# Kernel optimization log

Hardware: AMD Instinct MI355X
Metric: run time of the kernel (lower is better)

Reference implementation:

```python
import jax, jax.numpy as jnp
import numpy as np

N = 20000      # nodes
E = 320000     # edges (avg degree 16)
IN = 64        # input feature dim
EMB = 128      # emb_dim / c_dim
OUT = 10       # num classes
L = 5          # num_layers
RATIO = 0.25
TEMP = 1.0
NOISE = 1.0
MAX_ITER = 30
EPS = 1e-20


def setup_inputs() -> dict:
    key = jax.random.key(0)
    ks = jax.random.split(key, 12)
    def w(k, shape, fan):
        return jax.random.normal(k, shape, jnp.float32) / np.float32(np.sqrt(fan))
    x = jax.random.normal(ks[0], (N, IN), jnp.float32)
    edge_index = jax.random.randint(ks[1], (2, E), 0, N, jnp.int32)
    u = jax.random.uniform(ks[2], (E, 1), jnp.float32)
    return {
        "x": x,
        "edge_index": edge_index,
        "u": u,
        "enc_W0": w(ks[3], (IN, EMB), IN), "enc_b0": jnp.zeros((EMB,), jnp.float32),
        "enc_W": w(ks[4], (L - 1, EMB, EMB), EMB), "enc_b": jnp.zeros((L - 1, EMB), jnp.float32),
        "ea_W1": w(ks[5], (2 * EMB, 4 * EMB), 2 * EMB), "ea_b1": jnp.zeros((4 * EMB,), jnp.float32),
        "ea_W2": w(ks[6], (4 * EMB, 1), 4 * EMB), "ea_b2": jnp.zeros((1,), jnp.float32),
        "cls_W0": w(ks[7], (IN, EMB), IN), "cls_b0": jnp.zeros((EMB,), jnp.float32),
        "cls_W": w(ks[8], (L - 1, EMB, EMB), EMB), "cls_b": jnp.zeros((L - 1, EMB), jnp.float32),
        "head_W": w(ks[9], (EMB, OUT), EMB), "head_b": jnp.zeros((OUT,), jnp.float32),
    }


def _gin_stack(x, W0, b0, Ws, bs, src, dst, att):
    """GIN-style stack: aggregate att-weighted neighbor messages, then linear+ReLU."""
    agg = jax.ops.segment_sum(x[src] * att, dst, num_segments=N)
    h = jax.nn.relu((x + agg) @ W0 + b0)
    def layer(h, wb):
        W, b = wb
        agg = jax.ops.segment_sum(h[src] * att, dst, num_segments=N)
        return jax.nn.relu((h + agg) @ W + b), None
    h, _ = jax.lax.scan(layer, h, (Ws, bs))
    return h


def reference(x, edge_index, u, enc_W0, enc_b0, enc_W, enc_b,
              ea_W1, ea_b1, ea_W2, ea_b2,
              cls_W0, cls_b0, cls_W, cls_b, head_W, head_b):
    src, dst = edge_index[0], edge_index[1]
    ones = jnp.ones((E, 1), jnp.float32)

    # GNN encoder
    h = _gin_stack(x, enc_W0, enc_b0, enc_W, enc_b, src, dst, ones)

    # edge attention MLP on [h_src, h_dst]
    edge_rep = jnp.concatenate([h[src], h[dst]], axis=-1)            # [E, 2*EMB]
    pe = jax.nn.relu(edge_rep @ ea_W1 + ea_b1) @ ea_W2 + ea_b2       # [E, 1]
    atts = (pe - pe.mean()) / jnp.std(pe, ddof=1)

    # Gumbel noise from uniform u (training path)
    g = -jnp.log(-jnp.log(u + EPS) + EPS)
    d = atts + g * NOISE

    s_min, s_max = atts.min(), atts.max()
    D = jnp.concatenate([d - s_min, s_max - d], axis=-1)             # [E, 2]
    logT = -D / TEMP
    log_rs = jnp.log(jnp.array([[E * (1.0 - RATIO), E * RATIO]], jnp.float32) + EPS)

    # 30-step Sinkhorn normalization in log space
    def body(i, lt):
        lt = lt - jax.scipy.special.logsumexp(lt, axis=-1, keepdims=True)
        lt = lt - jax.scipy.special.logsumexp(lt, axis=-2, keepdims=True)
        return lt + log_rs
    logT = jax.lax.fori_loop(0, MAX_ITER, body, logT)
    T = jnp.exp(logT)[:, 1:2]                                        # [E, 1]

    # classifier GNN on raw features with Sinkhorn edge attention
    hc = _gin_stack(x, cls_W0, cls_b0, cls_W, cls_b, src, dst, T)
    rep = hc.mean(axis=0)                                            # mean graph pooling
    return rep @ head_W + head_b                                     # [OUT]
```

## Files before the change

### kernel.cpp

```cpp
#include <hip/hip_runtime.h>
#include <math.h>

#define NN 20000
#define EE 320000
#define NBINS 2048
#define HRANGE 64.0f
#define EPSF 1e-20f

typedef __attribute__((ext_vector_type(8))) short bf16x8;
typedef __attribute__((ext_vector_type(4))) float f32x4;

constexpr size_t OFF_DEG  = 0;
constexpr size_t OFF_RS   = 20000;
constexpr size_t OFF_CUR  = 40008;
constexpr size_t OFF_EIX  = 60008;
constexpr size_t OFF_GSRC = 380008;
constexpr size_t OFF_B0   = 700008;
constexpr size_t OFF_B1   = 1980008;
constexpr size_t OFF_PA   = 3260008;
constexpr size_t OFF_PB   = 8380008;
constexpr size_t OFF_PE   = 13500008;
constexpr size_t OFF_DL   = 13820008;
constexpr size_t OFF_TT   = 14140008;
constexpr size_t OFF_HIST = 14460008;
constexpr size_t OFF_SCAL = 14464104;
constexpr size_t OFF_REP  = 14464136;
constexpr size_t OFF_WT   = 14464264;
constexpr size_t WT_ENC0 = 0;
constexpr size_t WT_ENC  = 8192;
constexpr size_t WT_CLS0 = 73728;
constexpr size_t WT_CLS  = 81920;
constexpr size_t WT_EA1  = 147456;

__device__ __forceinline__ unsigned ordf(float f) {
  unsigned b = __float_as_uint(f);
  return (b >> 31) ? ~b : (b | 0x80000000u);
}
__device__ __forceinline__ float unordf(unsigned u) {
  unsigned b = (u >> 31) ? (u ^ 0x80000000u) : ~u;
  return __uint_as_float(b);
}
__device__ __forceinline__ ushort f2bf(float f) {
  unsigned u = __float_as_uint(f);
  u += 0x7FFFu + ((u >> 16) & 1u);
  return (ushort)(u >> 16);
}
__device__ __forceinline__ unsigned pack2(float x, float y) {
  return (unsigned)f2bf(x) | ((unsigned)f2bf(y) << 16);
}
__device__ __forceinline__ float bf2f(ushort h) {
  return __uint_as_float(((unsigned)h) << 16);
}
__device__ __forceinline__ float bflo(unsigned v) { return __uint_as_float(v << 16); }
__device__ __forceinline__ float bfhi(unsigned v) { return __uint_as_float(v & 0xFFFF0000u); }

__global__ void init_ws(int* deg, int* cur, float* hist, float* scal, float* rep) {
  int i = blockIdx.x * blockDim.x + threadIdx.x;
  if (i < NN) { deg[i] = 0; cur[i] = 0; }
  if (i < 2 * NBINS) hist[i] = 0.f;
  if (i < 128) rep[i] = 0.f;
  if (i < 32) {
    if (i == 2)      ((unsigned*)scal)[2] = 0xFFFFFFFFu;
    else if (i == 3) ((unsigned*)scal)[3] = 0u;
    else scal[i] = 0.f;
  }
}

__global__ void count_deg(const int* __restrict__ dst, int* __restrict__ deg) {
  int e = blockIdx.x * 256 + threadIdx.x;
  if (e < EE) atomicAdd(&deg[dst[e]], 1);
}

__global__ __launch_bounds__(1024) void scan_deg(const int* __restrict__ deg,
                                                 int* __restrict__ rs) {
  __shared__ int ps[1024];
  const int t = threadIdx.x;
  const int base = t * 20;
  int loc[20];
  int s = 0;
#pragma unroll
  for (int j = 0; j < 20; ++j) {
    int idx = base + j;
    int v = (idx < NN) ? deg[idx] : 0;
    loc[j] = s;
    s += v;
  }
  ps[t] = s;
  __syncthreads();
  for (int off = 1; off < 1024; off <<= 1) {
    int x = (t >= off) ? ps[t - off] : 0;
    __syncthreads();
    ps[t] += x;
    __syncthreads();
  }
  const int excl = ps[t] - s;
#pragma unroll
  for (int j = 0; j < 20; ++j) {
    int idx = base + j;
    if (idx < NN) rs[idx] = excl + loc[j];
  }
  if (t == 1023) rs[NN] = ps[1023];
}

__global__ void fill_csr(const int* __restrict__ src, const int* __restrict__ dst,
                         const int* __restrict__ rs, int* __restrict__ cur,
                         int* __restrict__ eidx, int* __restrict__ gsrc) {
  int e = blockIdx.x * 256 + threadIdx.x;
  if (e < EE) {
    int d = dst[e];
    int p = atomicAdd(&cur[d], 1);
    int o = rs[d] + p;
    eidx[o] = e;
    gsrc[o] = src[e];
  }
}

__global__ void transpose_all(const float* __restrict__ encW0, const float* __restrict__ encW,
                              const float* __restrict__ clsW0, const float* __restrict__ clsW,
                              const float* __restrict__ eaW1, ushort* __restrict__ Wt) {
  int i = blockIdx.x * 256 + threadIdx.x;
  if (i < 8192) {
    int k = i >> 7, n = i & 127;
    Wt[WT_ENC0 + n * 64 + k] = f2bf(encW0[i]);
  } else if (i < 73728) {
    int j = i - 8192;
    int l = j >> 14, r = j & 16383, k = r >> 7, n = r & 127;
    Wt[WT_ENC + l * 16384 + n * 128 + k] = f2bf(encW[j]);
  } else if (i < 81920) {
    int j = i - 73728;
    int k = j >> 7, n = j & 127;
    Wt[WT_CLS0 + n * 64 + k] = f2bf(clsW0[j]);
  } else if (i < 147456) {
    int j = i - 81920;
    int l = j >> 14, r = j & 16383, k = r >> 7, n = r & 127;
    Wt[WT_CLS + l * 16384 + n * 128 + k] = f2bf(clsW[j]);
  } else if (i < 278528) {
    int j = i - 147456;
    int k = j >> 9, n = j & 511;
    Wt[WT_EA1 + n * 256 + k] = f2bf(eaW1[j]);
  }
}

template <bool HASATT>
__global__ __launch_bounds__(256) void fused_layer64(
    const float* __restrict__ X, ushort* __restrict__ C,
    const int* __restrict__ gsrc, const int* __restrict__ rs,
    const float* __restrict__ att, const ushort* __restrict__ Bt,
    const float* __restrict__ bias) {
  __shared__ __align__(16) char smem[16896];
  ushort* Asm = (ushort*)smem;
  const int tid = threadIdx.x;
  const int g = tid >> 3, l = tid & 7;
  const int nb = blockIdx.x * 32;
  {
    const int n = nb + g;
    const int e0 = rs[n], e1 = rs[n + 1];
    const float4* Xr = (const float4*)(X + (size_t)n * 64);
    float4 s0 = Xr[l * 2], s1 = Xr[l * 2 + 1];
    float a[8] = {s0.x, s0.y, s0.z, s0.w, s1.x, s1.y, s1.z, s1.w};
    int i = e0;
    float4 c0, c1, d0, d1;
    float cw = 1.f, dw = 1.f;
    if (i < e1) {
      const float4* R = (const float4*)(X + (size_t)gsrc[i] * 64);
      if (HASATT) cw = att[i];
      c0 = R[l * 2]; c1 = R[l * 2 + 1];
    }
    if (i + 1 < e1) {
      const float4* R = (const float4*)(X + (size_t)gsrc[i + 1] * 64);
      if (HASATT) dw = att[i + 1];
      d0 = R[l * 2]; d1 = R[l * 2 + 1];
    }
    while (i < e1) {
      float4 p0, p1;
      float pw = 1.f;
      if (i + 2 < e1) {
        const float4* R = (const float4*)(X + (size_t)gsrc[i + 2] * 64);
        if (HASATT) pw = att[i + 2];
        p0 = R[l * 2]; p1 = R[l * 2 + 1];
      }
      a[0] = fmaf(cw, c0.x, a[0]); a[1] = fmaf(cw, c0.y, a[1]);
      a[2] = fmaf(cw, c0.z, a[2]); a[3] = fmaf(cw, c0.w, a[3]);
      a[4] = fmaf(cw, c1.x, a[4]); a[5] = fmaf(cw, c1.y, a[5]);
      a[6] = fmaf(cw, c1.z, a[6]); a[7] = fmaf(cw, c1.w, a[7]);
      c0 = d0; c1 = d1; cw = dw;
      d0 = p0; d1 = p1; dw = pw;
      ++i;
    }
    uint4 o;
    o.x = pack2(a[0], a[1]); o.y = pack2(a[2], a[3]);
    o.z = pack2(a[4], a[5]); o.w = pack2(a[6], a[7]);
    *(uint4*)(Asm + g * 80 + l * 8) = o;
  }
  __syncthreads();
  const int wave = tid >> 6, lane = tid & 63, quad = lane >> 4, l15 = lane & 15;
  const int mh = wave >> 1, nh = wave & 1;
  f32x4 acc[4] = {{0.f, 0.f, 0.f, 0.f}, {0.f, 0.f, 0.f, 0.f},
                  {0.f, 0.f, 0.f, 0.f}, {0.f, 0.f, 0.f, 0.f}};
#pragma unroll
  for (int k0 = 0; k0 < 64; k0 += 32) {
    bf16x8 af = *(const bf16x8*)(Asm + (mh * 16 + l15) * 80 + k0 + quad * 8);
#pragma unroll
    for (int t = 0; t < 4; ++t) {
      int bn = nh * 64 + t * 16 + l15;
      bf16x8 bf = *(const bf16x8*)(Bt + (size_t)bn * 64 + k0 + quad * 8);
      acc[t] = __builtin_amdgcn_mfma_f32_16x16x32_bf16(af, bf, acc[t], 0, 0, 0);
    }
  }
  __syncthreads();
  float (*Csm)[132] = (float(*)[132])smem;
#pragma unroll
  for (int t = 0; t < 4; ++t) {
    int lc = nh * 64 + t * 16 + l15;
    float bs = bias[lc];
#pragma unroll
    for (int r = 0; r < 4; ++r)
      Csm[mh * 16 + quad * 4 + r][lc] = fmaxf(acc[t][r] + bs, 0.f);
  }
  __syncthreads();
  const int r = tid >> 3, c0 = (tid & 7) * 16;
  ushort* Cp = C + (size_t)(nb + r) * 128 + c0;
#pragma unroll
  for (int k = 0; k < 4; ++k) {
    f32x4 vv = *(const f32x4*)&Csm[r][c0 + k * 4];
    ushort4 o;
    o.x = f2bf(vv[0]); o.y = f2bf(vv[1]); o.z = f2bf(vv[2]); o.w = f2bf(vv[3]);
    *(ushort4*)(Cp + k * 4) = o;
  }
}

template <bool HASATT>
__global__ __launch_bounds__(256) void fused_layer128(
    const ushort* __restrict__ Xb, ushort* __restrict__ C,
    const int* __restrict__ gsrc, const int* __restrict__ rs,
    const float* __restrict__ att, const ushort* __restrict__ Bt,
    const float* __restrict__ bias) {
  __shared__ __align__(16) char smem[16896];
  ushort* Asm = (ushort*)smem;
  const int tid = threadIdx.x;
  const int g = tid >> 3, l = tid & 7;
  const int nb = blockIdx.x * 32;
  {
    const int n = nb + g;
    const int e0 = rs[n], e1 = rs[n + 1];
    float a[16];
    {
      const uint4* Xr = (const uint4*)(Xb + (size_t)n * 128);
      uint4 s0 = Xr[l * 2], s1 = Xr[l * 2 + 1];
      a[0] = bflo(s0.x); a[1] = bfhi(s0.x); a[2] = bflo(s0.y); a[3] = bfhi(s0.y);
      a[4] = bflo(s0.z); a[5] = bfhi(s0.z); a[6] = bflo(s0.w); a[7] = bfhi(s0.w);
      a[8] = bflo(s1.x); a[9] = bfhi(s1.x); a[10] = bflo(s1.y); a[11] = bfhi(s1.y);
      a[12] = bflo(s1.z); a[13] = bfhi(s1.z); a[14] = bflo(s1.w); a[15] = bfhi(s1.w);
    }
    int i = e0;
    uint4 c0, c1, d0, d1;
    float cw = 1.f, dw = 1.f;
    if (i < e1) {
      const uint4* R = (const uint4*)(Xb + (size_t)gsrc[i] * 128);
      if (HASATT) cw = att[i];
      c0 = R[l * 2]; c1 = R[l * 2 + 1];
    }
    if (i + 1 < e1) {
      const uint4* R = (const uint4*)(Xb + (size_t)gsrc[i + 1] * 128);
      if (HASATT) dw = att[i + 1];
      d0 = R[l * 2]; d1 = R[l * 2 + 1];
    }
    while (i < e1) {
      uint4 p0, p1;
      float pw = 1.f;
      if (i + 2 < e1) {
        const uint4* R = (const uint4*)(Xb + (size_t)gsrc[i + 2] * 128);
        if (HASATT) pw = att[i + 2];
        p0 = R[l * 2]; p1 = R[l * 2 + 1];
      }
      a[0] = fmaf(cw, bflo(c0.x), a[0]);  a[1] = fmaf(cw, bfhi(c0.x), a[1]);
      a[2] = fmaf(cw, bflo(c0.y), a[2]);  a[3] = fmaf(cw, bfhi(c0.y), a[3]);
      a[4] = fmaf(cw, bflo(c0.z), a[4]);  a[5] = fmaf(cw, bfhi(c0.z), a[5]);
      a[6] = fmaf(cw, bflo(c0.w), a[6]);  a[7] = fmaf(cw, bfhi(c0.w), a[7]);
      a[8] = fmaf(cw, bflo(c1.x), a[8]);  a[9] = fmaf(cw, bfhi(c1.x), a[9]);
      a[10] = fmaf(cw, bflo(c1.y), a[10]); a[11] = fmaf(cw, bfhi(c1.y), a[11]);
      a[12] = fmaf(cw, bflo(c1.z), a[12]); a[13] = fmaf(cw, bfhi(c1.z), a[13]);
      a[14] = fmaf(cw, bflo(c1.w), a[14]); a[15] = fmaf(cw, bfhi(c1.w), a[15]);
      c0 = d0; c1 = d1; cw = dw;
      d0 = p0; d1 = p1; dw = pw;
      ++i;
    }
    uint4 o0, o1;
    o0.x = pack2(a[0], a[1]); o0.y = pack2(a[2], a[3]);
    o0.z = pack2(a[4], a[5]); o0.w = pack2(a[6], a[7]);
    o1.x = pack2(a[8], a[9]); o1.y = pack2(a[10], a[11]);
    o1.z = pack2(a[12], a[13]); o1.w = pack2(a[14], a[15]);
    *(uint4*)(Asm + g * 136 + l * 16) = o0;
    *(uint4*)(Asm + g * 136 + l * 16 + 8) = o1;
  }
  __syncthreads();
  const int wave = tid >> 6, lane = tid & 63, quad = lane >> 4, l15 = lane & 15;
  const int mh = wave >> 1, nh = wave & 1;
  f32x4 acc[4] = {{0.f, 0.f, 0.f, 0.f}, {0.f, 0.f, 0.f, 0.f},
                  {0.f, 0.f, 0.f, 0.f}, {0.f, 0.f, 0.f, 0.f}};
#pragma unroll
  for (int k0 = 0; k0 < 128; k0 += 32) {
    bf16x8 af = *(const bf16x8*)(Asm + (mh * 16 + l15) * 136 + k0 + quad * 8);
#pragma unroll
    for (int t = 0; t < 4; ++t) {
      int bn = nh * 64 + t * 16 + l15;
      bf16x8 bf = *(const bf16x8*)(Bt + (size_t)bn * 128 + k0 + quad * 8);
      acc[t] = __builtin_amdgcn_mfma_f32_16x16x32_bf16(af, bf, acc[t], 0, 0, 0);
    }
  }
  __syncthreads();
  float (*Csm)[132] = (float(*)[132])smem;
#pragma unroll
  for (int t = 0; t < 4; ++t) {
    int lc = nh * 64 + t * 16 + l15;
    float bs = bias[lc];
#pragma unroll
    for (int r = 0; r < 4; ++r)
      Csm[mh * 16 + quad * 4 + r][lc] = fmaxf(acc[t][r] + bs, 0.f);
  }
  __syncthreads();
  const int r = tid >> 3, c0 = (tid & 7) * 16;
  ushort* Cp = C + (size_t)(nb + r) * 128 + c0;
#pragma unroll
  for (int k = 0; k < 4; ++k) {
    f32x4 vv = *(const f32x4*)&Csm[r][c0 + k * 4];
    ushort4 o;
    o.x = f2bf(vv[0]); o.y = f2bf(vv[1]); o.z = f2bf(vv[2]); o.w = f2bf(vv[3]);
    *(ushort4*)(Cp + k * 4) = o;
  }
}

__global__ __launch_bounds__(256) void gemm_papb(
    const ushort* __restrict__ Hb, const ushort* __restrict__ W1t,
    const float* __restrict__ b1, ushort* __restrict__ Pa, ushort* __restrict__ Pb) {
  __shared__ float lds[32][132];
  const int tid = threadIdx.x;
  const int wave = tid >> 6, lane = tid & 63, quad = lane >> 4, l15 = lane & 15;
  const int mh = wave >> 1, nh = wave & 1;
  const bool isB = blockIdx.x >= 4;
  const int col0 = (blockIdx.x & 3) * 128;
  const int row0 = blockIdx.y * 32;
  const ushort* Bt = W1t + (isB ? 128 : 0);
  ushort* C = isB ? Pb : Pa;
  f32x4 acc[4] = {{0.f, 0.f, 0.f, 0.f}, {0.f, 0.f, 0.f, 0.f},
                  {0.f, 0.f, 0.f, 0.f}, {0.f, 0.f, 0.f, 0.f}};
  const ushort* Ap = Hb + (size_t)(row0 + mh * 16 + l15) * 128 + quad * 8;
#pragma unroll
  for (int k0 = 0; k0 < 128; k0 += 32) {
    bf16x8 af = *(const bf16x8*)(Ap + k0);
#pragma unroll
    for (int t = 0; t < 4; ++t) {
      int bn = col0 + nh * 64 + t * 16 + l15;
      bf16x8 bf = *(const bf16x8*)(Bt + (size_t)bn * 256 + k0 + quad * 8);
      acc[t] = __builtin_amdgcn_mfma_f32_16x16x32_bf16(af, bf, acc[t], 0, 0, 0);
    }
  }
#pragma unroll
  for (int t = 0; t < 4; ++t) {
    int lc = nh * 64 + t * 16 + l15;
    float bs = isB ? 0.f : b1[col0 + lc];
#pragma unroll
    for (int r = 0; r < 4; ++r)
      lds[mh * 16 + quad * 4 + r][lc] = acc[t][r] + bs;
  }
  __syncthreads();
  const int r = tid >> 3, c0 = (tid & 7) * 16;
  ushort* Cp = C + (size_t)(row0 + r) * 512 + col0 + c0;
#pragma unroll
  for (int k = 0; k < 4; ++k) {
    f32x4 v = *(const f32x4*)&lds[r][c0 + k * 4];
    ushort4 o;
    o.x = f2bf(v[0]); o.y = f2bf(v[1]); o.z = f2bf(v[2]); o.w = f2bf(v[3]);
    *(ushort4*)(Cp + k * 4) = o;
  }
}

__global__ __launch_bounds__(256) void edge_pe_csr(
    const ushort* __restrict__ Pa, const ushort* __restrict__ Pb,
    const int* __restrict__ gsrc, const int* __restrict__ rs,
    const float* __restrict__ W2, const float* __restrict__ b2,
    float* __restrict__ pe) {
  const int tid = threadIdx.x;
  const int lane = tid & 63;
  const int hl = lane & 31;
  const int n = blockIdx.x * 8 + (tid >> 5);
  if (n >= NN) return;
  const int e0 = rs[n], e1 = rs[n + 1];
  if (e0 == e1) return;
  float w[16], pb[16];
  {
    const float4* w2v = (const float4*)(W2 + hl * 16);
#pragma unroll
    for (int q = 0; q < 4; ++q) {
      float4 t = w2v[q];
      w[q * 4 + 0] = t.x; w[q * 4 + 1] = t.y; w[q * 4 + 2] = t.z; w[q * 4 + 3] = t.w;
    }
    const uint4* pbr = (const uint4*)(Pb + (size_t)n * 512);
    uint4 b0 = pbr[hl * 2], b1 = pbr[hl * 2 + 1];
    pb[0] = bflo(b0.x); pb[1] = bfhi(b0.x); pb[2] = bflo(b0.y); pb[3] = bfhi(b0.y);
    pb[4] = bflo(b0.z); pb[5] = bfhi(b0.z); pb[6] = bflo(b0.w); pb[7] = bfhi(b0.w);
    pb[8] = bflo(b1.x); pb[9] = bfhi(b1.x); pb[10] = bflo(b1.y); pb[11] = bfhi(b1.y);
    pb[12] = bflo(b1.z); pb[13] = bfhi(b1.z); pb[14] = bflo(b1.w); pb[15] = bfhi(b1.w);
  }
  const float b2v = b2[0];
  int i = e0;
  uint4 c0, c1, d0, d1;
  {
    const uint4* R = (const uint4*)(Pa + (size_t)gsrc[i] * 512);
    c0 = R[hl * 2]; c1 = R[hl * 2 + 1];
  }
  if (i + 1 < e1) {
    const uint4* R = (const uint4*)(Pa + (size_t)gsrc[i + 1] * 512);
    d0 = R[hl * 2]; d1 = R[hl * 2 + 1];
  }
  while (i < e1) {
    uint4 p0, p1;
    if (i + 2 < e1) {
      const uint4* R = (const uint4*)(Pa + (size_t)gsrc[i + 2] * 512);
      p0 = R[hl * 2]; p1 = R[hl * 2 + 1];
    }
    float pa[16] = {bflo(c0.x), bfhi(c0.x), bflo(c0.y), bfhi(c0.y),
                    bflo(c0.z), bfhi(c0.z), bflo(c0.w), bfhi(c0.w),
                    bflo(c1.x), bfhi(c1.x), bflo(c1.y), bfhi(c1.y),
                    bflo(c1.z), bfhi(c1.z), bflo(c1.w), bfhi(c1.w)};
    float acc = 0.f;
#pragma unroll
    for (int j = 0; j < 16; ++j) acc += fmaxf(pa[j] + pb[j], 0.f) * w[j];
#pragma unroll
    for (int off = 16; off; off >>= 1) acc += __shfl_xor(acc, off);
    if (hl == 0) pe[i] = acc + b2v;
    c0 = d0; c1 = d1;
    d0 = p0; d1 = p1;
    ++i;
  }
}

__global__ __launch_bounds__(256) void pe_stats(const float* __restrict__ pe,
                                                float* __restrict__ scal) {
  __shared__ float r1[256], r2[256], r3[256], r4[256];
  int tid = threadIdx.x;
  float s = 0.f, q = 0.f, mn = 3.0e38f, mx = -3.0e38f;
  for (int i = blockIdx.x * 256 + tid; i < EE; i += gridDim.x * 256) {
    float v = pe[i];
    s += v; q = fmaf(v, v, q);
    mn = fminf(mn, v); mx = fmaxf(mx, v);
  }
  r1[tid] = s; r2[tid] = q; r3[tid] = mn; r4[tid] = mx;
  __syncthreads();
  for (int k = 128; k > 0; k >>= 1) {
    if (tid < k) {
      r1[tid] += r1[tid + k];
      r2[tid] += r2[tid + k];
      r3[tid] = fminf(r3[tid], r3[tid + k]);
      r4[tid] = fmaxf(r4[tid], r4[tid + k]);
    }
    __syncthreads();
  }
  if (tid == 0) {
    unsafeAtomicAdd(&scal[0], r1[0]);
    unsafeAtomicAdd(&scal[1], r2[0]);
    atomicMin((unsigned*)scal + 2, ordf(r3[0]));
    atomicMax((unsigned*)scal + 3, ordf(r4[0]));
  }
}

__global__ __launch_bounds__(256) void edge_delta_hist(
    const float* __restrict__ pe, const float* __restrict__ u,
    const int* __restrict__ eidx, float* __restrict__ delta,
    float* __restrict__ hist, const float* __restrict__ scal) {
  __shared__ float cnt_s[NBINS], sum_s[NBINS];
  for (int b = threadIdx.x; b < NBINS; b += 256) { cnt_s[b] = 0.f; sum_s[b] = 0.f; }
  float sum = scal[0], ssq = scal[1];
  float mn = unordf(((const unsigned*)scal)[2]);
  float mx = unordf(((const unsigned*)scal)[3]);
  float mu = sum / (float)EE;
  float var = (ssq - sum * sum / (float)EE) / (float)(EE - 1);
  float istd = rsqrtf(fmaxf(var, 1e-30f));
  float shift = (mn - mu) * istd + (mx - mu) * istd;
  __syncthreads();
  for (int i = blockIdx.x * 256 + threadIdx.x; i < EE; i += gridDim.x * 256) {
    float uu = u[eidx[i]];
    float atts = (pe[i] - mu) * istd;
    float g = -logf(-logf(uu + EPSF) + EPSF);
    float dl = 2.0f * (atts + g) - shift;
    delta[i] = dl;
    float dcl = fminf(fmaxf(dl, -HRANGE), HRANGE * 0.9999f);
    int b = (int)((dcl + HRANGE) * ((float)NBINS / (2.0f * HRANGE)));
    b = min(max(b, 0), NBINS - 1);
    atomicAdd(&cnt_s[b], 1.0f);
    atomicAdd(&sum_s[b], dcl);
  }
  __syncthreads();
  for (int b = threadIdx.x; b < NBINS; b += 256) {
    float c = cnt_s[b];
    if (c != 0.f) {
      unsafeAtomicAdd(&hist[b], c);
      unsafeAtomicAdd(&hist[NBINS + b], sum_s[b]);
    }
  }
}

__global__ __launch_bounds__(64) void sinkhorn_iter(const float* __restrict__ hist,
                                                    float* __restrict__ scal) {
  const int lane = threadIdx.x;
  float cnt[32], mean[32];
#pragma unroll
  for (int b = 0; b < 32; ++b) {
    int idx = b * 64 + lane;
    float c = hist[idx];
    cnt[b] = c;
    mean[b] = (c > 0.f) ? hist[NBINS + idx] / c : 0.f;
  }
  const float LRD = -1.0986122886681098f;
  float S = 0.f, Zfin = 0.f;
  for (int it = 0; it < 30; ++it) {
    float p = 0.f;
#pragma unroll
    for (int b = 0; b < 32; ++b)
      if (cnt[b] > 0.f) p += cnt[b] / (1.f + expf(-(mean[b] + S)));
#pragma unroll
    for (int off = 32; off; off >>= 1) p += __shfl_xor(p, off);
    if (it < 29)
      S += logf(fmaxf((float)EE - p, 1.0f)) - logf(p) + LRD;
    else
      Zfin = p;
  }
  if (lane == 0) {
    scal[8] = S;
    scal[9] = ((float)EE * 0.25f) / Zfin;
  }
}

__global__ void compute_T(const float* __restrict__ delta,
                          const float* __restrict__ scal,
                          float* __restrict__ Ta) {
  int i = blockIdx.x * 256 + threadIdx.x;
  if (i >= EE) return;
  float S = scal[8], sc = scal[9];
  Ta[i] = sc / (1.f + expf(-(delta[i] + S)));
}

__global__ __launch_bounds__(128) void col_mean(const ushort* __restrict__ Hc,
                                                float* __restrict__ rep) {
  int c = threadIdx.x;
  const int g = gridDim.x;
  float p0 = 0.f, p1 = 0.f, p2 = 0.f, p3 = 0.f;
  int n = blockIdx.x;
  for (; n + 3 * g < NN; n += 4 * g) {
    p0 += bf2f(Hc[(size_t)n * 128 + c]);
    p1 += bf2f(Hc[(size_t)(n + g) * 128 + c]);
    p2 += bf2f(Hc[(size_t)(n + 2 * g) * 128 + c]);
    p3 += bf2f(Hc[(size_t)(n + 3 * g) * 128 + c]);
  }
  for (; n < NN; n += g) p0 += bf2f(Hc[(size_t)n * 128 + c]);
  unsafeAtomicAdd(&rep[c], (p0 + p1) + (p2 + p3));
}

__global__ __launch_bounds__(128) void head_kernel(const float* __restrict__ repsum,
                                                   const float* __restrict__ hW,
                                                   const float* __restrict__ hb,
                                                   float* __restrict__ out) {
  __shared__ float rep[128];
  int tid = threadIdx.x;
  if (tid < 128) rep[tid] = repsum[tid] * (1.0f / (float)NN);
  __syncthreads();
  if (tid < 10) {
    float a = hb[tid];
#pragma unroll
    for (int c = 0; c < 128; c++) a = fmaf(rep[c], hW[c * 10 + tid], a);
    out[tid] = a;
  }
}

extern "C" void kernel_launch(void* const* d_in, const int* in_sizes, int n_in,
                              void* d_out, int out_size, void* d_ws, size_t ws_size,
                              hipStream_t stream) {
  const float* x      = (const float*)d_in[0];
  const int*   ei     = (const int*)d_in[1];
  const float* u      = (const float*)d_in[2];
  const float* enc_W0 = (const float*)d_in[3];
  const float* enc_b0 = (const float*)d_in[4];
  const float* enc_W  = (const float*)d_in[5];
  const float* enc_b  = (const float*)d_in[6];
  const float* ea_W1  = (const float*)d_in[7];
  const float* ea_b1  = (const float*)d_in[8];
  const float* ea_W2  = (const float*)d_in[9];
  const float* ea_b2  = (const float*)d_in[10];
  const float* cls_W0 = (const float*)d_in[11];
  const float* cls_b0 = (const float*)d_in[12];
  const float* cls_W  = (const float*)d_in[13];
  const float* cls_b  = (const float*)d_in[14];
  const float* head_W = (const float*)d_in[15];
  const float* head_b = (const float*)d_in[16];
  const int* src  = ei;
  const int* dstp = ei + EE;

  float* wsF = (float*)d_ws;
  int*   wsI = (int*)d_ws;
  int* deg  = wsI + OFF_DEG;
  int* rs   = wsI + OFF_RS;
  int* cur  = wsI + OFF_CUR;
  int* eix  = wsI + OFF_EIX;
  int* gsrc = wsI + OFF_GSRC;
  ushort* B0 = (ushort*)(wsF + OFF_B0);
  ushort* B1 = (ushort*)(wsF + OFF_B1);
  ushort* Pa = (ushort*)(wsF + OFF_PA);
  ushort* Pb = (ushort*)(wsF + OFF_PB);
  float* pe   = wsF + OFF_PE;
  float* dl   = wsF + OFF_DL;
  float* Ta   = wsF + OFF_TT;
  float* hist = wsF + OFF_HIST;
  float* scal = wsF + OFF_SCAL;
  float* rep  = wsF + OFF_REP;
  ushort* Wt  = (ushort*)(wsF + OFF_WT);
  float* out = (float*)d_out;

  init_ws<<<(NN + 255) / 256, 256, 0, stream>>>(deg, cur, hist, scal, rep);
  count_deg<<<(EE + 255) / 256, 256, 0, stream>>>(dstp, deg);
  scan_deg<<<1, 1024, 0, stream>>>(deg, rs);
  fill_csr<<<(EE + 255) / 256, 256, 0, stream>>>(src, dstp, rs, cur, eix, gsrc);
  transpose_all<<<1088, 256, 0, stream>>>(enc_W0, enc_W, cls_W0, cls_W, ea_W1, Wt);

  const int GB = NN / 32;

  fused_layer64<false><<<GB, 256, 0, stream>>>(x, B0, gsrc, rs, nullptr, Wt + WT_ENC0, enc_b0);
  {
    ushort* in = B0; ushort* outb = B1;
    for (int l = 0; l < 4; l++) {
      fused_layer128<false><<<GB, 256, 0, stream>>>(in, outb, gsrc, rs, nullptr,
                                                    Wt + WT_ENC + (size_t)l * 16384,
                                                    enc_b + (size_t)l * 128);
      ushort* t = in; in = outb; outb = t;
    }
  }

  gemm_papb<<<dim3(8, GB), 256, 0, stream>>>(B0, Wt + WT_EA1, ea_b1, Pa, Pb);
  edge_pe_csr<<<NN / 8, 256, 0, stream>>>(Pa, Pb, gsrc, rs, ea_W2, ea_b2, pe);

  pe_stats<<<512, 256, 0, stream>>>(pe, scal);
  edge_delta_hist<<<128, 256, 0, stream>>>(pe, u, eix, dl, hist, scal);
  sinkhorn_iter<<<1, 64, 0, stream>>>(hist, scal);
  compute_T<<<(EE + 255) / 256, 256, 0, stream>>>(dl, scal, Ta);

  fused_layer64<true><<<GB, 256, 0, stream>>>(x, B0, gsrc, rs, Ta, Wt + WT_CLS0, cls_b0);
  {
    ushort* in = B0; ushort* outb = B1;
    for (int l = 0; l < 4; l++) {
      fused_layer128<true><<<GB, 256, 0, stream>>>(in, outb, gsrc, rs, Ta,
                                                   Wt + WT_CLS + (size_t)l * 16384,
                                                   cls_b + (size_t)l * 128);
      ushort* t = in; in = outb; outb = t;
    }
  }

  col_mean<<<256, 128, 0, stream>>>(B0, rep);
  head_kernel<<<1, 128, 0, stream>>>(rep, head_W, head_b, out);
}
```

Measured before the change: 613.6 us.

## Widen gather lanes per node and halve node tile in fused GIN layers

```diff
diff --git a/kernel.cpp b/kernel.cpp
--- a/kernel.cpp
+++ b/kernel.cpp
@@ -147,62 +147,53 @@
     const int* __restrict__ gsrc, const int* __restrict__ rs,
     const float* __restrict__ att, const ushort* __restrict__ Bt,
     const float* __restrict__ bias) {
-  __shared__ __align__(16) char smem[16896];
+  __shared__ __align__(16) char smem[8448];
   ushort* Asm = (ushort*)smem;
   const int tid = threadIdx.x;
-  const int g = tid >> 3, l = tid & 7;
-  const int nb = blockIdx.x * 32;
+  const int g = tid >> 4, l = tid & 15;
+  const int nb = blockIdx.x * 16;
   {
     const int n = nb + g;
     const int e0 = rs[n], e1 = rs[n + 1];
-    const float4* Xr = (const float4*)(X + (size_t)n * 64);
-    float4 s0 = Xr[l * 2], s1 = Xr[l * 2 + 1];
-    float a[8] = {s0.x, s0.y, s0.z, s0.w, s1.x, s1.y, s1.z, s1.w};
+    float4 s = ((const float4*)(X + (size_t)n * 64))[l];
+    float a[4] = {s.x, s.y, s.z, s.w};
     int i = e0;
-    float4 c0, c1, d0, d1;
+    float4 c, d;
     float cw = 1.f, dw = 1.f;
     if (i < e1) {
-      const float4* R = (const float4*)(X + (size_t)gsrc[i] * 64);
+      c = ((const float4*)(X + (size_t)gsrc[i] * 64))[l];
       if (HASATT) cw = att[i];
-      c0 = R[l * 2]; c1 = R[l * 2 + 1];
     }
     if (i + 1 < e1) {
-      const float4* R = (const float4*)(X + (size_t)gsrc[i + 1] * 64);
+      d = ((const float4*)(X + (size_t)gsrc[i + 1] * 64))[l];
       if (HASATT) dw = att[i + 1];
-      d0 = R[l * 2]; d1 = R[l * 2 + 1];
     }
     while (i < e1) {
-      float4 p0, p1;
+      float4 p;
       float pw = 1.f;
       if (i + 2 < e1) {
-        const float4* R = (const float4*)(X + (size_t)gsrc[i + 2] * 64);
+        p = ((const float4*)(X + (size_t)gsrc[i + 2] * 64))[l];
         if (HASATT) pw = att[i + 2];
-        p0 = R[l * 2]; p1 = R[l * 2 + 1];
       }
-      a[0] = fmaf(cw, c0.x, a[0]); a[1] = fmaf(cw, c0.y, a[1]);
-      a[2] = fmaf(cw, c0.z, a[2]); a[3] = fmaf(cw, c0.w, a[3]);
-      a[4] = fmaf(cw, c1.x, a[4]); a[5] = fmaf(cw, c1.y, a[5]);
-      a[6] = fmaf(cw, c1.z, a[6]); a[7] = fmaf(cw, c1.w, a[7]);
-      c0 = d0; c1 = d1; cw = dw;
-      d0 = p0; d1 = p1; dw = pw;
+      a[0] = fmaf(cw, c.x, a[0]); a[1] = fmaf(cw, c.y, a[1]);
+      a[2] = fmaf(cw, c.z, a[2]); a[3] = fmaf(cw, c.w, a[3]);
+      c = d; cw = dw;
+      d = p; dw = pw;
       ++i;
     }
-    uint4 o;
-    o.x = pack2(a[0], a[1]); o.y = pack2(a[2], a[3]);
-    o.z = pack2(a[4], a[5]); o.w = pack2(a[6], a[7]);
-    *(uint4*)(Asm + g * 80 + l * 8) = o;
+    ushort4 o;
+    o.x = f2bf(a[0]); o.y = f2bf(a[1]); o.z = f2bf(a[2]); o.w = f2bf(a[3]);
+    *(ushort4*)(Asm + g * 72 + l * 4) = o;
   }
   __syncthreads();
   const int wave = tid >> 6, lane = tid & 63, quad = lane >> 4, l15 = lane & 15;
-  const int mh = wave >> 1, nh = wave & 1;
-  f32x4 acc[4] = {{0.f, 0.f, 0.f, 0.f}, {0.f, 0.f, 0.f, 0.f},
-                  {0.f, 0.f, 0.f, 0.f}, {0.f, 0.f, 0.f, 0.f}};
+  f32x4 acc[2] = {{0.f, 0.f, 0.f, 0.f}, {0.f, 0.f, 0.f, 0.f}};
 #pragma unroll
   for (int k0 = 0; k0 < 64; k0 += 32) {
-    bf16x8 af = *(const bf16x8*)(Asm + (mh * 16 + l15) * 80 + k0 + quad * 8);
-#pragma unroll
-    for (int t = 0; t < 4; ++t) {
-      int bn = nh * 64 + t * 16 + l15;
+    bf16x8 af = *(const bf16x8*)(Asm + l15 * 72 + k0 + quad * 8);
+#pragma unroll
+    for (int t = 0; t < 2; ++t) {
+      int bn = wave * 32 + t * 16 + l15;
       bf16x8 bf = *(const bf16x8*)(Bt + (size_t)bn * 64 + k0 + quad * 8);
       acc[t] = __builtin_amdgcn_mfma_f32_16x16x32_bf16(af, bf, acc[t], 0, 0, 0);
     }
@@ -210,23 +201,21 @@
   __syncthreads();
   float (*Csm)[132] = (float(*)[132])smem;
 #pragma unroll
-  for (int t = 0; t < 4; ++t) {
-    int lc = nh * 64 + t * 16 + l15;
+  for (int t = 0; t < 2; ++t) {
+    int lc = wave * 32 + t * 16 + l15;
     float bs = bias[lc];
 #pragma unroll
     for (int r = 0; r < 4; ++r)
-      Csm[mh * 16 + quad * 4 + r][lc] = fmaxf(acc[t][r] + bs, 0.f);
-  }
-  __syncthreads();
-  const int r = tid >> 3, c0 = (tid & 7) * 16;
-  ushort* Cp = C + (size_t)(nb + r) * 128 + c0;
-#pragma unroll
-  for (int k = 0; k < 4; ++k) {
-    f32x4 vv = *(const f32x4*)&Csm[r][c0 + k * 4];
-    ushort4 o;
-    o.x = f2bf(vv[0]); o.y = f2bf(vv[1]); o.z = f2bf(vv[2]); o.w = f2bf(vv[3]);
-    *(ushort4*)(Cp + k * 4) = o;
-  }
+      Csm[quad * 4 + r][lc] = fmaxf(acc[t][r] + bs, 0.f);
+  }
+  __syncthreads();
+  const int r = tid >> 4, cc = (tid & 15) * 8;
+  f32x4 v0 = *(const f32x4*)&Csm[r][cc];
+  f32x4 v1 = *(const f32x4*)&Csm[r][cc + 4];
+  uint4 o;
+  o.x = pack2(v0[0], v0[1]); o.y = pack2(v0[2], v0[3]);
+  o.z = pack2(v1[0], v1[1]); o.w = pack2(v1[2], v1[3]);
+  *(uint4*)(C + (size_t)(nb + r) * 128 + cc) = o;
 }
 
 template <bool HASATT>
@@ -235,75 +224,60 @@
     const int* __restrict__ gsrc, const int* __restrict__ rs,
     const float* __restrict__ att, const ushort* __restrict__ Bt,
     const float* __restrict__ bias) {
-  __shared__ __align__(16) char smem[16896];
+  __shared__ __align__(16) char smem[8448];
   ushort* Asm = (ushort*)smem;
   const int tid = threadIdx.x;
-  const int g = tid >> 3, l = tid & 7;
-  const int nb = blockIdx.x * 32;
+  const int g = tid >> 4, l = tid & 15;
+  const int nb = blockIdx.x * 16;
   {
     const int n = nb + g;
     const int e0 = rs[n], e1 = rs[n + 1];
-    float a[16];
+    float a[8];
     {
-      const uint4* Xr = (const uint4*)(Xb + (size_t)n * 128);
-      uint4 s0 = Xr[l * 2], s1 = Xr[l * 2 + 1];
-      a[0] = bflo(s0.x); a[1] = bfhi(s0.x); a[2] = bflo(s0.y); a[3] = bfhi(s0.y);
-      a[4] = bflo(s0.z); a[5] = bfhi(s0.z); a[6] = bflo(s0.w); a[7] = bfhi(s0.w);
-      a[8] = bflo(s1.x); a[9] = bfhi(s1.x); a[10] = bflo(s1.y); a[11] = bfhi(s1.y);
-      a[12] = bflo(s1.z); a[13] = bfhi(s1.z); a[14] = bflo(s1.w); a[15] = bfhi(s1.w);
+      uint4 s = ((const uint4*)(Xb + (size_t)n * 128))[l];
+      a[0] = bflo(s.x); a[1] = bfhi(s.x); a[2] = bflo(s.y); a[3] = bfhi(s.y);
+      a[4] = bflo(s.z); a[5] = bfhi(s.z); a[6] = bflo(s.w); a[7] = bfhi(s.w);
     }
     int i = e0;
-    uint4 c0, c1, d0, d1;
+    uint4 c, d;
     float cw = 1.f, dw = 1.f;
     if (i < e1) {
-      const uint4* R = (const uint4*)(Xb + (size_t)gsrc[i] * 128);
+      c = ((const uint4*)(Xb + (size_t)gsrc[i] * 128))[l];
       if (HASATT) cw = att[i];
-      c0 = R[l * 2]; c1 = R[l * 2 + 1];
     }
     if (i + 1 < e1) {
-      const uint4* R = (const uint4*)(Xb + (size_t)gsrc[i + 1] * 128);
+      d = ((const uint4*)(Xb + (size_t)gsrc[i + 1] * 128))[l];
       if (HASATT) dw = att[i + 1];
-      d0 = R[l * 2]; d1 = R[l * 2 + 1];
     }
     while (i < e1) {
-      uint4 p0, p1;
+      uint4 p;
       float pw = 1.f;
       if (i + 2 < e1) {
-        const uint4* R = (const uint4*)(Xb + (size_t)gsrc[i + 2] * 128);
+        p = ((const uint4*)(Xb + (size_t)gsrc[i + 2] * 128))[l];
         if (HASATT) pw = att[i + 2];
-        p0 = R[l * 2]; p1 = R[l * 2 + 1];
       }
-      a[0] = fmaf(cw, bflo(c0.x), a[0]);  a[1] = fmaf(cw, bfhi(c0.x), a[1]);
-      a[2] = fmaf(cw, bflo(c0.y), a[2]);  a[3] = fmaf(cw, bfhi(c0.y), a[3]);
-      a[4] = fmaf(cw, bflo(c0.z), a[4]);  a[5] = fmaf(cw, bfhi(c0.z), a[5]);
-      a[6] = fmaf(cw, bflo(c0.w), a[6]);  a[7] = fmaf(cw, bfhi(c0.w), a[7]);
-      a[8] = fmaf(cw, bflo(c1.x), a[8]);  a[9] = fmaf(cw, bfhi(c1.x), a[9]);
-      a[10] = fmaf(cw, bflo(c1.y), a[10]); a[11] = fmaf(cw, bfhi(c1.y), a[11]);
-      a[12] = fmaf(cw, bflo(c1.z), a[12]); a[13] = fmaf(cw, bfhi(c1.z), a[13]);
-      a[14] = fmaf(cw, bflo(c1.w), a[14]); a[15] = fmaf(cw, bfhi(c1.w), a[15]);
-      c0 = d0; c1 = d1; cw = dw;
-      d0 = p0; d1 = p1; dw = pw;
+      a[0] = fmaf(cw, bflo(c.x), a[0]); a[1] = fmaf(cw, bfhi(c.x), a[1]);
+      a[2] = fmaf(cw, bflo(c.y), a[2]); a[3] = fmaf(cw, bfhi(c.y), a[3]);
+      a[4] = fmaf(cw, bflo(c.z), a[4]); a[5] = fmaf(cw, bfhi(c.z), a[5]);
+      a[6] = fmaf(cw, bflo(c.w), a[6]); a[7] = fmaf(cw, bfhi(c.w), a[7]);
+      c = d; cw = dw;
+      d = p; dw = pw;
       ++i;
     }
-    uint4 o0, o1;
-    o0.x = pack2(a[0], a[1]); o0.y = pack2(a[2], a[3]);
-    o0.z = pack2(a[4], a[5]); o0.w = pack2(a[6], a[7]);
-    o1.x = pack2(a[8], a[9]); o1.y = pack2(a[10], a[11]);
-    o1.z = pack2(a[12], a[13]); o1.w = pack2(a[14], a[15]);
-    *(uint4*)(Asm + g * 136 + l * 16) = o0;
-    *(uint4*)(Asm + g * 136 + l * 16 + 8) = o1;
+    uint4 o;
+    o.x = pack2(a[0], a[1]); o.y = pack2(a[2], a[3]);
+    o.z = pack2(a[4], a[5]); o.w = pack2(a[6], a[7]);
+    *(uint4*)(Asm + g * 136 + l * 8) = o;
   }
   __syncthreads();
   const int wave = tid >> 6, lane = tid & 63, quad = lane >> 4, l15 = lane & 15;
-  const int mh = wave >> 1, nh = wave & 1;
-  f32x4 acc[4] = {{0.f, 0.f, 0.f, 0.f}, {0.f, 0.f, 0.f, 0.f},
-                  {0.f, 0.f, 0.f, 0.f}, {0.f, 0.f, 0.f, 0.f}};
+  f32x4 acc[2] = {{0.f, 0.f, 0.f, 0.f}, {0.f, 0.f, 0.f, 0.f}};
 #pragma unroll
   for (int k0 = 0; k0 < 128; k0 += 32) {
-    bf16x8 af = *(const bf16x8*)(Asm + (mh * 16 + l15) * 136 + k0 + quad * 8);
-#pragma unroll
-    for (int t = 0; t < 4; ++t) {
-      int bn = nh * 64 + t * 16 + l15;
+    bf16x8 af = *(const bf16x8*)(Asm + l15 * 136 + k0 + quad * 8);
+#pragma unroll
+    for (int t = 0; t < 2; ++t) {
+      int bn = wave * 32 + t * 16 + l15;
       bf16x8 bf = *(const bf16x8*)(Bt + (size_t)bn * 128 + k0 + quad * 8);
       acc[t] = __builtin_amdgcn_mfma_f32_16x16x32_bf16(af, bf, acc[t], 0, 0, 0);
     }
@@ -311,23 +285,21 @@
   __syncthreads();
   float (*Csm)[132] = (float(*)[132])smem;
 #pragma unroll
-  for (int t = 0; t < 4; ++t) {
-    int lc = nh * 64 + t * 16 + l15;
+  for (int t = 0; t < 2; ++t) {
+    int lc = wave * 32 + t * 16 + l15;
     float bs = bias[lc];
 #pragma unroll
     for (int r = 0; r < 4; ++r)
-      Csm[mh * 16 + quad * 4 + r][lc] = fmaxf(acc[t][r] + bs, 0.f);
-  }
-  __syncthreads();
-  const int r = tid >> 3, c0 = (tid & 7) * 16;
-  ushort* Cp = C + (size_t)(nb + r) * 128 + c0;
-#pragma unroll
-  for (int k = 0; k < 4; ++k) {
-    f32x4 vv = *(const f32x4*)&Csm[r][c0 + k * 4];
-    ushort4 o;
-    o.x = f2bf(vv[0]); o.y = f2bf(vv[1]); o.z = f2bf(vv[2]); o.w = f2bf(vv[3]);
-    *(ushort4*)(Cp + k * 4) = o;
-  }
+      Csm[quad * 4 + r][lc] = fmaxf(acc[t][r] + bs, 0.f);
+  }
+  __syncthreads();
+  const int r = tid >> 4, cc = (tid & 15) * 8;
+  f32x4 v0 = *(const f32x4*)&Csm[r][cc];
+  f32x4 v1 = *(const f32x4*)&Csm[r][cc + 4];
+  uint4 o;
+  o.x = pack2(v0[0], v0[1]); o.y = pack2(v0[2], v0[3]);
+  o.z = pack2(v1[0], v1[1]); o.w = pack2(v1[2], v1[3]);
+  *(uint4*)(C + (size_t)(nb + r) * 128 + cc) = o;
 }
 
 __global__ __launch_bounds__(256) void gemm_papb(
@@ -380,57 +352,38 @@
     const int* __restrict__ gsrc, const int* __restrict__ rs,
     const float* __restrict__ W2, const float* __restrict__ b2,
     float* __restrict__ pe) {
-  const int tid = threadIdx.x;
-  const int lane = tid & 63;
-  const int hl = lane & 31;
-  const int n = blockIdx.x * 8 + (tid >> 5);
-  if (n >= NN) return;
+  const int lane = threadIdx.x & 63;
+  const int n = blockIdx.x * 4 + (threadIdx.x >> 6);
   const int e0 = rs[n], e1 = rs[n + 1];
   if (e0 == e1) return;
-  float w[16], pb[16];
+  float w[8], pb[8];
   {
-    const float4* w2v = (const float4*)(W2 + hl * 16);
-#pragma unroll
-    for (int q = 0; q < 4; ++q) {
-      float4 t = w2v[q];
-      w[q * 4 + 0] = t.x; w[q * 4 + 1] = t.y; w[q * 4 + 2] = t.z; w[q * 4 + 3] = t.w;
-    }
-    const uint4* pbr = (const uint4*)(Pb + (size_t)n * 512);
-    uint4 b0 = pbr[hl * 2], b1 = pbr[hl * 2 + 1];
-    pb[0] = bflo(b0.x); pb[1] = bfhi(b0.x); pb[2] = bflo(b0.y); pb[3] = bfhi(b0.y);
-    pb[4] = bflo(b0.z); pb[5] = bfhi(b0.z); pb[6] = bflo(b0.w); pb[7] = bfhi(b0.w);
-    pb[8] = bflo(b1.x); pb[9] = bfhi(b1.x); pb[10] = bflo(b1.y); pb[11] = bfhi(b1.y);
-    pb[12] = bflo(b1.z); pb[13] = bfhi(b1.z); pb[14] = bflo(b1.w); pb[15] = bfhi(b1.w);
+    const float4* w2v = (const float4*)(W2 + lane * 8);
+    float4 t0 = w2v[0], t1 = w2v[1];
+    w[0] = t0.x; w[1] = t0.y; w[2] = t0.z; w[3] = t0.w;
+    w[4] = t1.x; w[5] = t1.y; w[6] = t1.z; w[7] = t1.w;
+    uint4 b = ((const uint4*)(Pb + (size_t)n * 512))[lane];
+    pb[0] = bflo(b.x); pb[1] = bfhi(b.x); pb[2] = bflo(b.y); pb[3] = bfhi(b.y);
+    pb[4] = bflo(b.z); pb[5] = bfhi(b.z); pb[6] = bflo(b.w); pb[7] = bfhi(b.w);
   }
   const float b2v = b2[0];
   int i = e0;
-  uint4 c0, c1, d0, d1;
-  {
-    const uint4* R = (const uint4*)(Pa + (size_t)gsrc[i] * 512);
-    c0 = R[hl * 2]; c1 = R[hl * 2 + 1];
-  }
-  if (i + 1 < e1) {
-    const uint4* R = (const uint4*)(Pa + (size_t)gsrc[i + 1] * 512);
-    d0 = R[hl * 2]; d1 = R[hl * 2 + 1];
-  }
+  uint4 c, d;
+  c = ((const uint4*)(Pa + (size_t)gsrc[i] * 512))[lane];
+  if (i + 1 < e1) d = ((const uint4*)(Pa + (size_t)gsrc[i + 1] * 512))[lane];
   while (i < e1) {
-    uint4 p0, p1;
-    if (i + 2 < e1) {
-      const uint4* R = (const uint4*)(Pa + (size_t)gsrc[i + 2] * 512);
-      p0 = R[hl * 2]; p1 = R[hl * 2 + 1];
-    }
-    float pa[16] = {bflo(c0.x), bfhi(c0.x), bflo(c0.y), bfhi(c0.y),
-                    bflo(c0.z), bfhi(c0.z), bflo(c0.w), bfhi(c0.w),
-                    bflo(c1.x), bfhi(c1.x), bflo(c1.y), bfhi(c1.y),
-                    bflo(c1.z), bfhi(c1.z), bflo(c1.w), bfhi(c1.w)};
+    uint4 p;
+    if (i + 2 < e1) p = ((const uint4*)(Pa + (size_t)gsrc[i + 2] * 512))[lane];
+    float pa[8] = {bflo(c.x), bfhi(c.x), bflo(c.y), bfhi(c.y),
+                   bflo(c.z), bfhi(c.z), bflo(c.w), bfhi(c.w)};
     float acc = 0.f;
 #pragma unroll
-    for (int j = 0; j < 16; ++j) acc += fmaxf(pa[j] + pb[j], 0.f) * w[j];
-#pragma unroll
-    for (int off = 16; off; off >>= 1) acc += __shfl_xor(acc, off);
-    if (hl == 0) pe[i] = acc + b2v;
-    c0 = d0; c1 = d1;
-    d0 = p0; d1 = p1;
+    for (int j = 0; j < 8; ++j) acc += fmaxf(pa[j] + pb[j], 0.f) * w[j];
+#pragma unroll
+    for (int off = 32; off; off >>= 1) acc += __shfl_xor(acc, off);
+    if (lane == 0) pe[i] = acc + b2v;
+    c = d;
+    d = p;
     ++i;
   }
 }
@@ -621,7 +574,7 @@
   fill_csr<<<(EE + 255) / 256, 256, 0, stream>>>(src, dstp, rs, cur, eix, gsrc);
   transpose_all<<<1088, 256, 0, stream>>>(enc_W0, enc_W, cls_W0, cls_W, ea_W1, Wt);
 
-  const int GB = NN / 32;
+  const int GB = NN / 16;
 
   fused_layer64<false><<<GB, 256, 0, stream>>>(x, B0, gsrc, rs, nullptr, Wt + WT_ENC0, enc_b0);
   {
@@ -634,8 +587,8 @@
     }
   }
 
-  gemm_papb<<<dim3(8, GB), 256, 0, stream>>>(B0, Wt + WT_EA1, ea_b1, Pa, Pb);
-  edge_pe_csr<<<NN / 8, 256, 0, stream>>>(Pa, Pb, gsrc, rs, ea_W2, ea_b2, pe);
+  gemm_papb<<<dim3(8, NN / 32), 256, 0, stream>>>(B0, Wt + WT_EA1, ea_b1, Pa, Pb);
+  edge_pe_csr<<<NN / 4, 256, 0, stream>>>(Pa, Pb, gsrc, rs, ea_W2, ea_b2, pe);
 
   pe_stats<<<512, 256, 0, stream>>>(pe, scal);
   edge_delta_hist<<<128, 256, 0, stream>>>(pe, u, eix, dl, hist, scal);
```

Result: no change. 601.8 us (-1.9%).
